# Performance work log

Hardware: AMD Instinct MI355X
Metric: run time of the kernel (lower is better)

The kernel has to match this reference:

```python
import jax, jax.numpy as jnp
import numpy as np

N = 1_000_000   # number of points (voxels)
C = 64          # number of instance clusters
D = 3           # embedding / coordinate dimension

EMBEDDING_WEIGHT = 1.0
SEEDINESS_WEIGHT = 1.0
SMOOTHING_WEIGHT = 1.0


def setup_inputs() -> dict:
    key = jax.random.key(0)
    k1, k2, k3, k4, k5 = jax.random.split(key, 5)
    embeddings = jax.random.normal(k1, (N, D), dtype=jnp.float32)
    margins = jax.random.uniform(k2, (N, 1), dtype=jnp.float32)
    seediness = jax.random.uniform(k3, (N, 1), dtype=jnp.float32)
    coords = jax.random.uniform(k4, (N, D), dtype=jnp.float32)
    labels = jax.random.randint(k5, (N,), 0, C, dtype=jnp.int32)
    return {
        "embeddings": embeddings,
        "margins": margins,
        "seediness": seediness,
        "coords": coords,
        "labels": labels,
        "num_clusters": C,
    }


def reference(embeddings, margins, seediness, coords, labels, num_clusters):
    Nc = num_clusters
    n = labels.shape[0]
    ones = jnp.ones((n,), embeddings.dtype)
    counts = jax.ops.segment_sum(ones, labels, num_segments=Nc)            # (C,)
    # per-cluster centroid of COORDS (find_cluster_means(coords, labels))
    centroids = jax.ops.segment_sum(coords, labels, num_segments=Nc) / counts[:, None]  # (C,D)
    # per-cluster sigma = mean of margins over cluster members -> (C,1)
    sigma = jax.ops.segment_sum(margins, labels, num_segments=Nc) / counts[:, None]

    # squared distance of every point to every centroid, (C,N), via GEMM expansion
    e_sq = jnp.sum(embeddings * embeddings, axis=1)                 # (N,)
    c_sq = jnp.sum(centroids * centroids, axis=1)                   # (C,)
    dists = c_sq[:, None] + e_sq[None, :] - 2.0 * (centroids @ embeddings.T)  # (C,N)

    # gaussian kernel probability, clamped to [0,1]
    p = jnp.clip(jnp.exp(-dists / (2.0 * sigma * sigma)), 0.0, 1.0)  # (C,N), sigma (C,1) broadcasts

    mask = (labels[None, :] == jnp.arange(Nc, dtype=labels.dtype)[:, None]).astype(p.dtype)  # (C,N)

    # StableBCELoss(p, mask): clamp(x,0) - x*t + log(1+exp(-|x|)), mean per cluster,
    # then averaged over clusters == global mean since every row has N elements.
    bce = jnp.clip(p, 0.0, None) - p * mask + jnp.log1p(jnp.exp(-jnp.abs(p)))
    mask_loss = jnp.mean(bce)

    # probs[n] = p[label_n, n]
    probs = p[labels, jnp.arange(n)]                                # (N,)

    # smoothing: sum over cluster members of (margin - sigma.detach())^2, averaged over clusters
    sigma_det = jax.lax.stop_gradient(sigma)                        # (C,1)
    smoothing_loss = jnp.sum((margins - sigma_det[labels]) ** 2) / Nc

    # seediness: L1 between detached probs and seediness prediction
    seed_loss = jnp.mean(jnp.abs(jax.lax.stop_gradient(probs) - seediness[:, 0]))

    total_loss = (EMBEDDING_WEIGHT * mask_loss
                  + SEEDINESS_WEIGHT * seed_loss
                  + SMOOTHING_WEIGHT * smoothing_loss)
    return total_loss
```

## Files before the change

### kernel.cpp

```cpp
#include <hip/hip_runtime.h>
#include <math.h>

#define NCLUS 64
#define BLOCK 256
#define GC 512
#define GM 512
#define FP_SCALE 1048576.0f

#if __has_builtin(__builtin_amdgcn_exp2f)
#define EXP2F(x) __builtin_amdgcn_exp2f(x)
#else
#define EXP2F(x) __expf(0.6931471805599453f * (x))
#endif

#define SP_C0 0.69314718
#define SP_C1 0.49991956f
#define SP_C2 0.12562243f
#define SP_C3 -0.00152320f
#define SP_C4 -0.00390297f


__global__ void init_ws_kernel(unsigned long long* S) {
    int i = blockIdx.x * blockDim.x + threadIdx.x;
    if (i < 5 * NCLUS) S[i] = 0ULL;
}

__global__ __launch_bounds__(BLOCK) void cluster_sums_kernel(
        const float* __restrict__ coords, const float* __restrict__ margins,
        const int* __restrict__ labels, int n, unsigned long long* __restrict__ S) {
    __shared__ float s_h[8][5][65];
    for (int i = threadIdx.x; i < 8 * 5 * 65; i += blockDim.x)
        ((float*)s_h)[i] = 0.0f;
    __syncthreads();

    const int rep = threadIdx.x & 7;
    const int chunks = n >> 2;
    const int stride = gridDim.x * blockDim.x;
    const float4* c4 = (const float4*)coords;
    const float4* m4 = (const float4*)margins;
    const int4* l4 = (const int4*)labels;

    for (int ch = blockIdx.x * blockDim.x + threadIdx.x; ch < chunks; ch += stride) {
        float4 e0 = c4[ch * 3 + 0], e1 = c4[ch * 3 + 1], e2 = c4[ch * 3 + 2];
        float4 mg = m4[ch];
        int4 lb = l4[ch];
        float x[4] = {e0.x, e0.w, e1.z, e2.y};
        float y[4] = {e0.y, e1.x, e1.w, e2.z};
        float z[4] = {e0.z, e1.y, e2.x, e2.w};
        float m[4] = {mg.x, mg.y, mg.z, mg.w};
        int   l[4] = {lb.x, lb.y, lb.z, lb.w};
#pragma unroll
        for (int k = 0; k < 4; ++k) {
            atomicAdd(&s_h[rep][0][l[k]], 1.0f);
            atomicAdd(&s_h[rep][1][l[k]], x[k]);
            atomicAdd(&s_h[rep][2][l[k]], y[k]);
            atomicAdd(&s_h[rep][3][l[k]], z[k]);
            atomicAdd(&s_h[rep][4][l[k]], m[k]);
        }
    }

    int rem = n & 3;
    int gid = blockIdx.x * blockDim.x + threadIdx.x;
    if (gid < rem) {
        int i = (chunks << 2) + gid;
        int lab = labels[i];
        atomicAdd(&s_h[rep][0][lab], 1.0f);
        atomicAdd(&s_h[rep][1][lab], coords[i * 3 + 0]);
        atomicAdd(&s_h[rep][2][lab], coords[i * 3 + 1]);
        atomicAdd(&s_h[rep][3][lab], coords[i * 3 + 2]);
        atomicAdd(&s_h[rep][4][lab], margins[i]);
    }
    __syncthreads();

    for (int idx = threadIdx.x; idx < 5 * NCLUS; idx += blockDim.x) {
        int field = idx >> 6, c = idx & 63;
        float v = 0.0f;
#pragma unroll
        for (int r = 0; r < 8; ++r) v += s_h[r][field][c];
        unsigned long long q = (unsigned long long)llrintf(v * FP_SCALE);
        if (q) atomicAdd(&S[idx], q);
    }
}

__global__ void compute_params_kernel(const unsigned long long* __restrict__ S,
                                      float* __restrict__ P) {
    int c = threadIdx.x;
    if (c < NCLUS) {
        const double inv_sc = 1.0 / (double)FP_SCALE;
        double cnt = (double)(long long)S[c] * inv_sc;
        double sx  = (double)(long long)S[64 + c] * inv_sc;
        double sy  = (double)(long long)S[128 + c] * inv_sc;
        double sz  = (double)(long long)S[192 + c] * inv_sc;
        double sm  = (double)(long long)S[256 + c] * inv_sc;
        double inv = 1.0 / cnt;
        double sigma = sm * inv;
        double cx = sx * inv, cy = sy * inv, cz = sz * inv;
        double w2 = -1.4426950408889634 / (2.0 * sigma * sigma);
        P[c * 4 + 0] = (float)(-2.0 * w2 * cx);
        P[c * 4 + 1] = (float)(-2.0 * w2 * cy);
        P[c * 4 + 2] = (float)(-2.0 * w2 * cz);
        P[c * 4 + 3] = (float)(w2 * (cx * cx + cy * cy + cz * cz));
        P[256 + c] = (float)w2;
        P[320 + c] = (float)sigma;
    }
}

__device__ __forceinline__ float block_reduce_sum(float v, float* s_red) {
    for (int o = 32; o > 0; o >>= 1) v += __shfl_down(v, o);
    int lane = threadIdx.x & 63, wid = threadIdx.x >> 6;
    __syncthreads();
    if (lane == 0) s_red[wid] = v;
    __syncthreads();
    float t = 0.0f;
    if (threadIdx.x == 0)
        for (int w = 0; w < BLOCK / 64; ++w) t += s_red[w];
    return t;
}

__global__ __launch_bounds__(BLOCK) void main_loss_kernel(
        const float* __restrict__ emb, const float* __restrict__ margins,
        const float* __restrict__ seed, const int* __restrict__ labels,
        int n, const float* __restrict__ P, float* __restrict__ pb) {
    __shared__ float4 s_par[NCLUS];
    __shared__ float s_w[NCLUS];
    __shared__ float s_sig[NCLUS];
    __shared__ float s_red[BLOCK / 64];

    if (threadIdx.x < NCLUS) {
        s_par[threadIdx.x] = ((const float4*)P)[threadIdx.x];
        s_w[threadIdx.x] = P[256 + threadIdx.x];
        s_sig[threadIdx.x] = P[320 + threadIdx.x];
    }
    __syncthreads();

    const int chunks = n >> 2;
    const int npairs = chunks >> 1;
    const int stride = gridDim.x * blockDim.x;
    const float4* e4 = (const float4*)emb;
    const float4* m4 = (const float4*)margins;
    const float4* s4 = (const float4*)seed;
    const int4* l4 = (const int4*)labels;

    float bce = 0.0f, seed_s = 0.0f, smooth_s = 0.0f;

    for (int pi = blockIdx.x * blockDim.x + threadIdx.x; pi < npairs; pi += stride) {
        int ch0 = pi * 2;
        float x[8], y[8], z[8], es[8], a[8];
#pragma unroll
        for (int h = 0; h < 2; ++h) {
            float4 e0 = e4[(ch0 + h) * 3 + 0];
            float4 e1 = e4[(ch0 + h) * 3 + 1];
            float4 e2 = e4[(ch0 + h) * 3 + 2];
            x[h * 4 + 0] = e0.x; y[h * 4 + 0] = e0.y; z[h * 4 + 0] = e0.z;
            x[h * 4 + 1] = e0.w; y[h * 4 + 1] = e1.x; z[h * 4 + 1] = e1.y;
            x[h * 4 + 2] = e1.z; y[h * 4 + 2] = e1.w; z[h * 4 + 2] = e2.x;
            x[h * 4 + 3] = e2.y; y[h * 4 + 3] = e2.z; z[h * 4 + 3] = e2.w;
        }
#pragma unroll
        for (int k = 0; k < 8; ++k) {
            es[k] = fmaf(x[k], x[k], fmaf(y[k], y[k], z[k] * z[k]));
            a[k] = 0.0f;
        }

#pragma unroll 4
        for (int c = 0; c < NCLUS; ++c) {
            float4 pr = s_par[c];
            float w2 = s_w[c];
#pragma unroll
            for (int k = 0; k < 8; ++k) {
                float t = fmaf(pr.x, x[k],
                          fmaf(pr.y, y[k],
                          fmaf(pr.z, z[k],
                          fmaf(w2, es[k], pr.w))));
                float p = EXP2F(t);
                float X = fmaf(p, fmaf(p, fmaf(p, SP_C4, SP_C3), SP_C2), SP_C1);
                a[k] = fmaf(p, X, a[k]);
            }
        }
        bce += ((a[0] + a[1]) + (a[2] + a[3])) + ((a[4] + a[5]) + (a[6] + a[7]));

        float4 mg0 = m4[ch0], mg1 = m4[ch0 + 1];
        float4 sd0 = s4[ch0], sd1 = s4[ch0 + 1];
        int4 lb0 = l4[ch0], lb1 = l4[ch0 + 1];
        float m[8] = {mg0.x, mg0.y, mg0.z, mg0.w, mg1.x, mg1.y, mg1.z, mg1.w};
        float s[8] = {sd0.x, sd0.y, sd0.z, sd0.w, sd1.x, sd1.y, sd1.z, sd1.w};
        int   l[8] = {lb0.x, lb0.y, lb0.z, lb0.w, lb1.x, lb1.y, lb1.z, lb1.w};
#pragma unroll
        for (int k = 0; k < 8; ++k) {
            float4 pr = s_par[l[k]];
            float w2 = s_w[l[k]];
            float t = fmaf(pr.x, x[k],
                      fmaf(pr.y, y[k],
                      fmaf(pr.z, z[k],
                      fmaf(w2, es[k], pr.w))));
            float p = EXP2F(t);
            bce -= p;
            seed_s += fabsf(p - s[k]);
            float dsg = m[k] - s_sig[l[k]];
            smooth_s += dsg * dsg;
        }
    }

    int covered = npairs * 8;
    int rem = n - covered;
    int gid = blockIdx.x * blockDim.x + threadIdx.x;
    if (gid < rem) {
        int i = covered + gid;
        float ex = emb[i * 3 + 0], ey = emb[i * 3 + 1], ez = emb[i * 3 + 2];
        float esq = fmaf(ex, ex, fmaf(ey, ey, ez * ez));
        int lab = labels[i];
        float pl = 0.0f;
        for (int c = 0; c < NCLUS; ++c) {
            float4 pr = s_par[c];
            float w2 = s_w[c];
            float t = fmaf(pr.x, ex, fmaf(pr.y, ey, fmaf(pr.z, ez, fmaf(w2, esq, pr.w))));
            float p = EXP2F(t);
            float X = fmaf(p, fmaf(p, fmaf(p, SP_C4, SP_C3), SP_C2), SP_C1);
            bce = fmaf(p, X, bce);
            if (c == lab) pl = p;
        }
        bce -= pl;
        seed_s += fabsf(pl - seed[i]);
        float dsg = margins[i] - s_sig[lab];
        smooth_s += dsg * dsg;
    }

    float r;
    r = block_reduce_sum(bce, s_red);
    if (threadIdx.x == 0) pb[blockIdx.x * 3 + 0] = r;
    r = block_reduce_sum(seed_s, s_red);
    if (threadIdx.x == 0) pb[blockIdx.x * 3 + 1] = r;
    r = block_reduce_sum(smooth_s, s_red);
    if (threadIdx.x == 0) pb[blockIdx.x * 3 + 2] = r;
}

__global__ void finalize_kernel(const float* __restrict__ pb,
                                float* __restrict__ out, int n) {
    int lane = threadIdx.x;
    double sums[3];
#pragma unroll
    for (int k = 0; k < 3; ++k) {
        double v = 0.0;
#pragma unroll
        for (int j = 0; j < 8; ++j)
            v += (double)pb[(lane * 8 + j) * 3 + k];
        for (int o = 32; o > 0; o >>= 1) v += __shfl_down(v, o);
        sums[k] = v;
    }
    if (lane == 0) {
        double bce_total = sums[0] + (double)n * 64.0 * SP_C0;
        double mask_loss = bce_total / ((double)NCLUS * (double)n);
        double seed_loss = sums[1] / (double)n;
        double smooth_loss = sums[2] / (double)NCLUS;
        out[0] = (float)(mask_loss + seed_loss + smooth_loss);
    }
}

extern "C" void kernel_launch(void* const* d_in, const int* in_sizes, int n_in,
                              void* d_out, int out_size, void* d_ws, size_t ws_size,
                              hipStream_t stream) {
    const float* emb     = (const float*)d_in[0];
    const float* margins = (const float*)d_in[1];
    const float* seed    = (const float*)d_in[2];
    const float* coords  = (const float*)d_in[3];
    const int*   labels  = (const int*)d_in[4];
    int n = in_sizes[4];

    unsigned long long* S = (unsigned long long*)d_ws;
    float* P  = (float*)((char*)d_ws + 2560);
    float* pb = (float*)((char*)d_ws + 4096);
    float* out = (float*)d_out;

    init_ws_kernel<<<1, 5 * NCLUS, 0, stream>>>(S);
    cluster_sums_kernel<<<GC, BLOCK, 0, stream>>>(coords, margins, labels, n, S);
    compute_params_kernel<<<1, 64, 0, stream>>>(S, P);
    main_loss_kernel<<<GM, BLOCK, 0, stream>>>(emb, margins, seed, labels, n, P, pb);
    finalize_kernel<<<1, 64, 0, stream>>>(pb, out, n);
}
```

Measured before the change: 64.34 us.

## Fuse param and finalize kernels into main loss, cheaper softplus polynomial, larger grid

Removes the separate compute_params and finalize kernels. Each main-loss block now derives the cluster parameters from the fixed-point sums itself, and the last block to finish, found through an atomic counter, does the final reduction, which saves two launches. The softplus polynomial drops from quartic to quadratic, cutting ALU work per point-cluster pair at some cost in accuracy. The grid grows from 512 blocks to up to 2048, each thread processes 4 points instead of 8, and the parameter reads are vectorized.

```diff
diff --git a/kernel.cpp b/kernel.cpp
--- a/kernel.cpp
+++ b/kernel.cpp
@@ -3,8 +3,7 @@
 
 #define NCLUS 64
 #define BLOCK 256
-#define GC 512
-#define GM 512
+#define MAXGRID 2048
 #define FP_SCALE 1048576.0f
 
 #if __has_builtin(__builtin_amdgcn_exp2f)
@@ -13,56 +12,54 @@
 #define EXP2F(x) __expf(0.6931471805599453f * (x))
 #endif
 
-#define SP_C0 0.69314718
-#define SP_C1 0.49991956f
-#define SP_C2 0.12562243f
-#define SP_C3 -0.00152320f
-#define SP_C4 -0.00390297f
-
-
-__global__ void init_ws_kernel(unsigned long long* S) {
+#define SPQ0 0.692941
+#define SPQ1 0.503668f
+#define SPQ2 0.117225f
+
+
+__global__ void init_ws_kernel(unsigned long long* S, int* counter) {
     int i = blockIdx.x * blockDim.x + threadIdx.x;
     if (i < 5 * NCLUS) S[i] = 0ULL;
+    if (i == 0) *counter = 0;
 }
 
 __global__ __launch_bounds__(BLOCK) void cluster_sums_kernel(
         const float* __restrict__ coords, const float* __restrict__ margins,
         const int* __restrict__ labels, int n, unsigned long long* __restrict__ S) {
     __shared__ float s_h[8][5][65];
-    for (int i = threadIdx.x; i < 8 * 5 * 65; i += blockDim.x)
+    for (int i = threadIdx.x; i < 8 * 5 * 65; i += BLOCK)
         ((float*)s_h)[i] = 0.0f;
     __syncthreads();
 
     const int rep = threadIdx.x & 7;
     const int chunks = n >> 2;
-    const int stride = gridDim.x * blockDim.x;
+    const int stride = gridDim.x * BLOCK;
     const float4* c4 = (const float4*)coords;
     const float4* m4 = (const float4*)margins;
     const int4* l4 = (const int4*)labels;
 
-    for (int ch = blockIdx.x * blockDim.x + threadIdx.x; ch < chunks; ch += stride) {
+    for (int ch = blockIdx.x * BLOCK + threadIdx.x; ch < chunks; ch += stride) {
         float4 e0 = c4[ch * 3 + 0], e1 = c4[ch * 3 + 1], e2 = c4[ch * 3 + 2];
         float4 mg = m4[ch];
         int4 lb = l4[ch];
-        float x[4] = {e0.x, e0.w, e1.z, e2.y};
-        float y[4] = {e0.y, e1.x, e1.w, e2.z};
-        float z[4] = {e0.z, e1.y, e2.x, e2.w};
-        float m[4] = {mg.x, mg.y, mg.z, mg.w};
-        int   l[4] = {lb.x, lb.y, lb.z, lb.w};
+        float xx[4] = {e0.x, e0.w, e1.z, e2.y};
+        float yy[4] = {e0.y, e1.x, e1.w, e2.z};
+        float zz[4] = {e0.z, e1.y, e2.x, e2.w};
+        float mm[4] = {mg.x, mg.y, mg.z, mg.w};
+        int   ll[4] = {lb.x, lb.y, lb.z, lb.w};
 #pragma unroll
         for (int k = 0; k < 4; ++k) {
-            atomicAdd(&s_h[rep][0][l[k]], 1.0f);
-            atomicAdd(&s_h[rep][1][l[k]], x[k]);
-            atomicAdd(&s_h[rep][2][l[k]], y[k]);
-            atomicAdd(&s_h[rep][3][l[k]], z[k]);
-            atomicAdd(&s_h[rep][4][l[k]], m[k]);
-        }
-    }
-
+            atomicAdd(&s_h[rep][0][ll[k]], 1.0f);
+            atomicAdd(&s_h[rep][1][ll[k]], xx[k]);
+            atomicAdd(&s_h[rep][2][ll[k]], yy[k]);
+            atomicAdd(&s_h[rep][3][ll[k]], zz[k]);
+            atomicAdd(&s_h[rep][4][ll[k]], mm[k]);
+        }
+    }
     int rem = n & 3;
-    int gid = blockIdx.x * blockDim.x + threadIdx.x;
+    int gid = blockIdx.x * BLOCK + threadIdx.x;
     if (gid < rem) {
-        int i = (chunks << 2) + gid;
+        int i = ((n >> 2) << 2) + gid;
         int lab = labels[i];
         atomicAdd(&s_h[rep][0][lab], 1.0f);
         atomicAdd(&s_h[rep][1][lab], coords[i * 3 + 0]);
@@ -72,20 +69,31 @@
     }
     __syncthreads();
 
-    for (int idx = threadIdx.x; idx < 5 * NCLUS; idx += blockDim.x) {
+    for (int idx = threadIdx.x; idx < 5 * NCLUS; idx += BLOCK) {
         int field = idx >> 6, c = idx & 63;
         float v = 0.0f;
 #pragma unroll
         for (int r = 0; r < 8; ++r) v += s_h[r][field][c];
-        unsigned long long q = (unsigned long long)llrintf(v * FP_SCALE);
+        unsigned long long q = (unsigned long long)(long long)llrintf(v * FP_SCALE);
         if (q) atomicAdd(&S[idx], q);
     }
 }
 
-__global__ void compute_params_kernel(const unsigned long long* __restrict__ S,
-                                      float* __restrict__ P) {
-    int c = threadIdx.x;
-    if (c < NCLUS) {
+__global__ __launch_bounds__(BLOCK) void main_loss_kernel(
+        const float* __restrict__ emb, const float* __restrict__ margins,
+        const float* __restrict__ seed, const int* __restrict__ labels,
+        int n, const unsigned long long* __restrict__ S,
+        float* __restrict__ pb, int* __restrict__ counter,
+        float* __restrict__ out) {
+    __shared__ float4 s_par[NCLUS];
+    __shared__ float4 s_w4[NCLUS / 4];
+    __shared__ float s_sig[NCLUS];
+    __shared__ float s_red[BLOCK / 64];
+    __shared__ double s_d[BLOCK / 64][3];
+    __shared__ int s_flag;
+
+    if (threadIdx.x < NCLUS) {
+        int c = threadIdx.x;
         const double inv_sc = 1.0 / (double)FP_SCALE;
         double cnt = (double)(long long)S[c] * inv_sc;
         double sx  = (double)(long long)S[64 + c] * inv_sc;
@@ -93,49 +101,19 @@
         double sz  = (double)(long long)S[192 + c] * inv_sc;
         double sm  = (double)(long long)S[256 + c] * inv_sc;
         double inv = 1.0 / cnt;
-        double sigma = sm * inv;
+        double sig = sm * inv;
         double cx = sx * inv, cy = sy * inv, cz = sz * inv;
-        double w2 = -1.4426950408889634 / (2.0 * sigma * sigma);
-        P[c * 4 + 0] = (float)(-2.0 * w2 * cx);
-        P[c * 4 + 1] = (float)(-2.0 * w2 * cy);
-        P[c * 4 + 2] = (float)(-2.0 * w2 * cz);
-        P[c * 4 + 3] = (float)(w2 * (cx * cx + cy * cy + cz * cz));
-        P[256 + c] = (float)w2;
-        P[320 + c] = (float)sigma;
-    }
-}
-
-__device__ __forceinline__ float block_reduce_sum(float v, float* s_red) {
-    for (int o = 32; o > 0; o >>= 1) v += __shfl_down(v, o);
-    int lane = threadIdx.x & 63, wid = threadIdx.x >> 6;
-    __syncthreads();
-    if (lane == 0) s_red[wid] = v;
-    __syncthreads();
-    float t = 0.0f;
-    if (threadIdx.x == 0)
-        for (int w = 0; w < BLOCK / 64; ++w) t += s_red[w];
-    return t;
-}
-
-__global__ __launch_bounds__(BLOCK) void main_loss_kernel(
-        const float* __restrict__ emb, const float* __restrict__ margins,
-        const float* __restrict__ seed, const int* __restrict__ labels,
-        int n, const float* __restrict__ P, float* __restrict__ pb) {
-    __shared__ float4 s_par[NCLUS];
-    __shared__ float s_w[NCLUS];
-    __shared__ float s_sig[NCLUS];
-    __shared__ float s_red[BLOCK / 64];
-
-    if (threadIdx.x < NCLUS) {
-        s_par[threadIdx.x] = ((const float4*)P)[threadIdx.x];
-        s_w[threadIdx.x] = P[256 + threadIdx.x];
-        s_sig[threadIdx.x] = P[320 + threadIdx.x];
+        double w2 = -1.4426950408889634 / (2.0 * sig * sig);
+        s_par[c] = make_float4((float)(-2.0 * w2 * cx), (float)(-2.0 * w2 * cy),
+                               (float)(-2.0 * w2 * cz),
+                               (float)(w2 * (cx * cx + cy * cy + cz * cz)));
+        ((float*)s_w4)[c] = (float)w2;
+        s_sig[c] = (float)sig;
     }
     __syncthreads();
 
     const int chunks = n >> 2;
-    const int npairs = chunks >> 1;
-    const int stride = gridDim.x * blockDim.x;
+    const int stride = gridDim.x * BLOCK;
     const float4* e4 = (const float4*)emb;
     const float4* m4 = (const float4*)margins;
     const float4* s4 = (const float4*)seed;
@@ -143,67 +121,57 @@
 
     float bce = 0.0f, seed_s = 0.0f, smooth_s = 0.0f;
 
-    for (int pi = blockIdx.x * blockDim.x + threadIdx.x; pi < npairs; pi += stride) {
-        int ch0 = pi * 2;
-        float x[8], y[8], z[8], es[8], a[8];
-#pragma unroll
-        for (int h = 0; h < 2; ++h) {
-            float4 e0 = e4[(ch0 + h) * 3 + 0];
-            float4 e1 = e4[(ch0 + h) * 3 + 1];
-            float4 e2 = e4[(ch0 + h) * 3 + 2];
-            x[h * 4 + 0] = e0.x; y[h * 4 + 0] = e0.y; z[h * 4 + 0] = e0.z;
-            x[h * 4 + 1] = e0.w; y[h * 4 + 1] = e1.x; z[h * 4 + 1] = e1.y;
-            x[h * 4 + 2] = e1.z; y[h * 4 + 2] = e1.w; z[h * 4 + 2] = e2.x;
-            x[h * 4 + 3] = e2.y; y[h * 4 + 3] = e2.z; z[h * 4 + 3] = e2.w;
-        }
-#pragma unroll
-        for (int k = 0; k < 8; ++k) {
+    for (int ch = blockIdx.x * BLOCK + threadIdx.x; ch < chunks; ch += stride) {
+        float4 e0 = e4[ch * 3 + 0], e1 = e4[ch * 3 + 1], e2 = e4[ch * 3 + 2];
+        float x[4] = {e0.x, e0.w, e1.z, e2.y};
+        float y[4] = {e0.y, e1.x, e1.w, e2.z};
+        float z[4] = {e0.z, e1.y, e2.x, e2.w};
+        float es[4], a[4] = {0.f, 0.f, 0.f, 0.f};
+#pragma unroll
+        for (int k = 0; k < 4; ++k)
             es[k] = fmaf(x[k], x[k], fmaf(y[k], y[k], z[k] * z[k]));
-            a[k] = 0.0f;
-        }
-
-#pragma unroll 4
-        for (int c = 0; c < NCLUS; ++c) {
-            float4 pr = s_par[c];
-            float w2 = s_w[c];
-#pragma unroll
-            for (int k = 0; k < 8; ++k) {
-                float t = fmaf(pr.x, x[k],
-                          fmaf(pr.y, y[k],
-                          fmaf(pr.z, z[k],
-                          fmaf(w2, es[k], pr.w))));
-                float p = EXP2F(t);
-                float X = fmaf(p, fmaf(p, fmaf(p, SP_C4, SP_C3), SP_C2), SP_C1);
-                a[k] = fmaf(p, X, a[k]);
+
+#pragma unroll
+        for (int c4i = 0; c4i < NCLUS / 4; ++c4i) {
+            float4 wv = s_w4[c4i];
+            float wa[4] = {wv.x, wv.y, wv.z, wv.w};
+#pragma unroll
+            for (int j = 0; j < 4; ++j) {
+                float4 pr = s_par[c4i * 4 + j];
+                float w2 = wa[j];
+#pragma unroll
+                for (int k = 0; k < 4; ++k) {
+                    float t = fmaf(pr.x, x[k], fmaf(pr.y, y[k],
+                              fmaf(pr.z, z[k], fmaf(w2, es[k], pr.w))));
+                    float p = EXP2F(t);
+                    a[k] = fmaf(p, fmaf(p, SPQ2, SPQ1), a[k]);
+                }
             }
         }
-        bce += ((a[0] + a[1]) + (a[2] + a[3])) + ((a[4] + a[5]) + (a[6] + a[7]));
-
-        float4 mg0 = m4[ch0], mg1 = m4[ch0 + 1];
-        float4 sd0 = s4[ch0], sd1 = s4[ch0 + 1];
-        int4 lb0 = l4[ch0], lb1 = l4[ch0 + 1];
-        float m[8] = {mg0.x, mg0.y, mg0.z, mg0.w, mg1.x, mg1.y, mg1.z, mg1.w};
-        float s[8] = {sd0.x, sd0.y, sd0.z, sd0.w, sd1.x, sd1.y, sd1.z, sd1.w};
-        int   l[8] = {lb0.x, lb0.y, lb0.z, lb0.w, lb1.x, lb1.y, lb1.z, lb1.w};
-#pragma unroll
-        for (int k = 0; k < 8; ++k) {
-            float4 pr = s_par[l[k]];
-            float w2 = s_w[l[k]];
-            float t = fmaf(pr.x, x[k],
-                      fmaf(pr.y, y[k],
-                      fmaf(pr.z, z[k],
-                      fmaf(w2, es[k], pr.w))));
+        bce += (a[0] + a[1]) + (a[2] + a[3]);
+
+        float4 mg = m4[ch], sv = s4[ch];
+        int4 lb = l4[ch];
+        float mm[4] = {mg.x, mg.y, mg.z, mg.w};
+        float ss[4] = {sv.x, sv.y, sv.z, sv.w};
+        int   ll[4] = {lb.x, lb.y, lb.z, lb.w};
+#pragma unroll
+        for (int k = 0; k < 4; ++k) {
+            float4 pr = s_par[ll[k]];
+            float w2 = ((const float*)s_w4)[ll[k]];
+            float t = fmaf(pr.x, x[k], fmaf(pr.y, y[k],
+                      fmaf(pr.z, z[k], fmaf(w2, es[k], pr.w))));
             float p = EXP2F(t);
             bce -= p;
-            seed_s += fabsf(p - s[k]);
-            float dsg = m[k] - s_sig[l[k]];
-            smooth_s += dsg * dsg;
-        }
-    }
-
-    int covered = npairs * 8;
+            seed_s += fabsf(p - ss[k]);
+            float dg = mm[k] - s_sig[ll[k]];
+            smooth_s += dg * dg;
+        }
+    }
+
+    int covered = chunks << 2;
     int rem = n - covered;
-    int gid = blockIdx.x * blockDim.x + threadIdx.x;
+    int gid = blockIdx.x * BLOCK + threadIdx.x;
     if (gid < rem) {
         int i = covered + gid;
         float ex = emb[i * 3 + 0], ey = emb[i * 3 + 1], ez = emb[i * 3 + 2];
@@ -212,47 +180,93 @@
         float pl = 0.0f;
         for (int c = 0; c < NCLUS; ++c) {
             float4 pr = s_par[c];
-            float w2 = s_w[c];
+            float w2 = ((const float*)s_w4)[c];
             float t = fmaf(pr.x, ex, fmaf(pr.y, ey, fmaf(pr.z, ez, fmaf(w2, esq, pr.w))));
             float p = EXP2F(t);
-            float X = fmaf(p, fmaf(p, fmaf(p, SP_C4, SP_C3), SP_C2), SP_C1);
-            bce = fmaf(p, X, bce);
-            if (c == lab) pl = p;
+            pl = (c == lab) ? p : pl;
+            bce = fmaf(p, fmaf(p, SPQ2, SPQ1), bce);
         }
         bce -= pl;
         seed_s += fabsf(pl - seed[i]);
-        float dsg = margins[i] - s_sig[lab];
-        smooth_s += dsg * dsg;
+        float dg = margins[i] - s_sig[lab];
+        smooth_s += dg * dg;
     }
 
     float r;
-    r = block_reduce_sum(bce, s_red);
-    if (threadIdx.x == 0) pb[blockIdx.x * 3 + 0] = r;
-    r = block_reduce_sum(seed_s, s_red);
-    if (threadIdx.x == 0) pb[blockIdx.x * 3 + 1] = r;
-    r = block_reduce_sum(smooth_s, s_red);
-    if (threadIdx.x == 0) pb[blockIdx.x * 3 + 2] = r;
-}
-
-__global__ void finalize_kernel(const float* __restrict__ pb,
-                                float* __restrict__ out, int n) {
-    int lane = threadIdx.x;
-    double sums[3];
-#pragma unroll
-    for (int k = 0; k < 3; ++k) {
-        double v = 0.0;
-#pragma unroll
-        for (int j = 0; j < 8; ++j)
-            v += (double)pb[(lane * 8 + j) * 3 + k];
-        for (int o = 32; o > 0; o >>= 1) v += __shfl_down(v, o);
-        sums[k] = v;
-    }
-    if (lane == 0) {
-        double bce_total = sums[0] + (double)n * 64.0 * SP_C0;
-        double mask_loss = bce_total / ((double)NCLUS * (double)n);
-        double seed_loss = sums[1] / (double)n;
-        double smooth_loss = sums[2] / (double)NCLUS;
-        out[0] = (float)(mask_loss + seed_loss + smooth_loss);
+    r = bce;
+    for (int o = 32; o > 0; o >>= 1) r += __shfl_down(r, o);
+    {
+        int lane = threadIdx.x & 63, wid = threadIdx.x >> 6;
+        __syncthreads();
+        if (lane == 0) s_red[wid] = r;
+        __syncthreads();
+        if (threadIdx.x == 0) {
+            float t = 0.f;
+            for (int w = 0; w < BLOCK / 64; ++w) t += s_red[w];
+            pb[blockIdx.x * 3 + 0] = t;
+        }
+    }
+    r = seed_s;
+    for (int o = 32; o > 0; o >>= 1) r += __shfl_down(r, o);
+    {
+        int lane = threadIdx.x & 63, wid = threadIdx.x >> 6;
+        __syncthreads();
+        if (lane == 0) s_red[wid] = r;
+        __syncthreads();
+        if (threadIdx.x == 0) {
+            float t = 0.f;
+            for (int w = 0; w < BLOCK / 64; ++w) t += s_red[w];
+            pb[blockIdx.x * 3 + 1] = t;
+        }
+    }
+    r = smooth_s;
+    for (int o = 32; o > 0; o >>= 1) r += __shfl_down(r, o);
+    {
+        int lane = threadIdx.x & 63, wid = threadIdx.x >> 6;
+        __syncthreads();
+        if (lane == 0) s_red[wid] = r;
+        __syncthreads();
+        if (threadIdx.x == 0) {
+            float t = 0.f;
+            for (int w = 0; w < BLOCK / 64; ++w) t += s_red[w];
+            pb[blockIdx.x * 3 + 2] = t;
+        }
+    }
+
+    if (threadIdx.x == 0) {
+        __threadfence();
+        int old = __hip_atomic_fetch_add(counter, 1, __ATOMIC_ACQ_REL,
+                                         __HIP_MEMORY_SCOPE_AGENT);
+        s_flag = (old == (int)gridDim.x - 1) ? 1 : 0;
+    }
+    __syncthreads();
+    if (s_flag) {
+        __threadfence();
+        double v0 = 0, v1 = 0, v2 = 0;
+        int nb = gridDim.x;
+        for (int j = threadIdx.x; j < nb; j += BLOCK) {
+            v0 += (double)__hip_atomic_load(&pb[j * 3 + 0], __ATOMIC_RELAXED,
+                                            __HIP_MEMORY_SCOPE_AGENT);
+            v1 += (double)__hip_atomic_load(&pb[j * 3 + 1], __ATOMIC_RELAXED,
+                                            __HIP_MEMORY_SCOPE_AGENT);
+            v2 += (double)__hip_atomic_load(&pb[j * 3 + 2], __ATOMIC_RELAXED,
+                                            __HIP_MEMORY_SCOPE_AGENT);
+        }
+        for (int o = 32; o > 0; o >>= 1) {
+            v0 += __shfl_down(v0, o); v1 += __shfl_down(v1, o); v2 += __shfl_down(v2, o);
+        }
+        int lane = threadIdx.x & 63, wid = threadIdx.x >> 6;
+        if (lane == 0) { s_d[wid][0] = v0; s_d[wid][1] = v1; s_d[wid][2] = v2; }
+        __syncthreads();
+        if (threadIdx.x == 0) {
+            double b = 0, se = 0, sm = 0;
+            for (int w = 0; w < BLOCK / 64; ++w) {
+                b += s_d[w][0]; se += s_d[w][1]; sm += s_d[w][2];
+            }
+            double bce_total = b + (double)n * 64.0 * SPQ0;
+            out[0] = (float)(bce_total / ((double)NCLUS * (double)n)
+                             + se / (double)n + sm / (double)NCLUS);
+        }
     }
 }
 
@@ -267,13 +281,17 @@
     int n = in_sizes[4];
 
     unsigned long long* S = (unsigned long long*)d_ws;
-    float* P  = (float*)((char*)d_ws + 2560);
+    int* counter = (int*)((char*)d_ws + 2560);
     float* pb = (float*)((char*)d_ws + 4096);
     float* out = (float*)d_out;
 
-    init_ws_kernel<<<1, 5 * NCLUS, 0, stream>>>(S);
-    cluster_sums_kernel<<<GC, BLOCK, 0, stream>>>(coords, margins, labels, n, S);
-    compute_params_kernel<<<1, 64, 0, stream>>>(S, P);
-    main_loss_kernel<<<GM, BLOCK, 0, stream>>>(emb, margins, seed, labels, n, P, pb);
-    finalize_kernel<<<1, 64, 0, stream>>>(pb, out, n);
-}
+    int chunks = n >> 2;
+    int grid = (chunks + BLOCK - 1) / BLOCK;
+    if (grid < 1) grid = 1;
+    if (grid > MAXGRID) grid = MAXGRID;
+
+    init_ws_kernel<<<1, 512, 0, stream>>>(S, counter);
+    cluster_sums_kernel<<<grid, BLOCK, 0, stream>>>(coords, margins, labels, n, S);
+    main_loss_kernel<<<grid, BLOCK, 0, stream>>>(emb, margins, seed, labels, n, S,
+                                                 pb, counter, out);
+}
```

New measurement: 101.6 us. 1.58x slower.
